# Kernel tuning notes

Measured on AMD Instinct MI355X. Metric: run time of the kernel, lower is better.

Reference implementation:

```python
import jax, jax.numpy as jnp
import numpy as np

IN_COUNT = 1024
OUT_COUNT = 1024
NUM_BASIS = 8
INPUT_ABS_MAX = 1.0
X_MIN = 0.0
X_MAX = 1.0
GAMMA_SCALE = 3.0
BATCH = 4096


def setup_inputs() -> dict:
    key = jax.random.key(0)
    k_x, k_c = jax.random.split(key)
    x = jax.random.normal(k_x, (BATCH, IN_COUNT), dtype=jnp.float32)
    coeffs = 0.01 * jax.random.normal(k_c, (OUT_COUNT, IN_COUNT, NUM_BASIS), dtype=jnp.float32)
    # fixed buffers
    centers_1d = jnp.linspace(X_MIN, X_MAX, NUM_BASIS)
    centers = jnp.broadcast_to(centers_1d[None, :], (IN_COUNT, NUM_BASIS)).astype(jnp.float32)
    delta = (X_MAX - X_MIN) / (NUM_BASIS - 1)
    gamma = GAMMA_SCALE / delta
    slopes = jnp.full((IN_COUNT, NUM_BASIS), gamma, dtype=jnp.float32)
    alpha = jnp.full((IN_COUNT,), (X_MAX - X_MIN) / (2.0 * INPUT_ABS_MAX), dtype=jnp.float32)
    beta = jnp.full((IN_COUNT,), 0.5 * (X_MIN + X_MAX), dtype=jnp.float32)
    return {"x": x, "coeffs": coeffs, "centers": centers, "slopes": slopes, "alpha": alpha, "beta": beta}


def reference(x, coeffs, centers, slopes, alpha, beta):
    # u: (B, in) affine transform with fixed alpha/beta
    u = alpha[None, :] * x + beta[None, :]
    # basis: (B, in, basis) = 0.5*(1+tanh(slope*(u - center)))
    basis = 0.5 * (1.0 + jnp.tanh(slopes[None, :, :] * (u[:, :, None] - centers[None, :, :])))
    # y[b,o] = sum_{i,m} coeffs[o,i,m] * basis[b,i,m]  (fused GEMM over in*basis)
    y = jnp.einsum('bim,oim->bo', basis, coeffs)
    return y
```

## Files before the change

### kernel.cpp

```cpp
#include <hip/hip_runtime.h>
#include <hip/hip_bf16.h>
#include <cstdint>
#include <cstddef>

#define BATCH 4096
#define INC   1024
#define OUTC  1024
#define NB    8
#define KDIM  (INC * NB)

#define BM 256
#define BN 256
#define BKB 64
#define SPLITS 4
#define KZ (KDIM / SPLITS)
#define KSTEPS (KZ / BKB)
#define GRID_BLOCKS ((OUTC / BN) * (BATCH / BM) * SPLITS)
#define FRAG (16 * BKB)

#define EXPAND_BLOCKS  ((BATCH * INC) / 256)
#define QUANT_BLOCKS   OUTC
#define PREP_BLOCKS    (EXPAND_BLOCKS + QUANT_BLOCKS)

typedef int      v4i __attribute__((ext_vector_type(4)));
typedef unsigned v4u __attribute__((ext_vector_type(4)));
typedef char     v8c __attribute__((ext_vector_type(8)));

__device__ __forceinline__ unsigned short f2bf(float f) {
  union { float f; unsigned u; } v; v.f = f;
  unsigned r = v.u + 0x7fffu + ((v.u >> 16) & 1u);
  return (unsigned short)(r >> 16);
}
__device__ __forceinline__ float bf2f(unsigned short h) {
  union { unsigned u; float f; } v; v.u = ((unsigned)h) << 16; return v.f;
}

__global__ __launch_bounds__(256) void prep_kernel(
    const float* __restrict__ x, const float4* __restrict__ coeffs4,
    const float* __restrict__ centers, const float* __restrict__ slopes,
    const float* __restrict__ alpha, const float* __restrict__ beta,
    char* __restrict__ Ai8, int* __restrict__ Ci8i,
    float* __restrict__ maxrow, int* __restrict__ qcsum) {
  const int blk = blockIdx.x;
  const int tid = threadIdx.x;
  if (blk < EXPAND_BLOCKS) {
    const int idx = blk * 256 + tid;
    const int i = idx & (INC - 1);
    const float u = alpha[i] * x[idx] + beta[i];
    const float s0 = slopes[i * NB];
    const float c0 = centers[i * NB];
    const float c1 = centers[i * NB + 1];
    const float L2E2 = 2.8853900817779268f;
    const float a2 = L2E2 * s0;
    float e = __builtin_amdgcn_exp2f(a2 * (c0 - u));
    const float R = __builtin_amdgcn_exp2f(a2 * (c1 - c0));
    v8c q;
#pragma unroll
    for (int m = 0; m < 8; ++m) {
      float basis = __builtin_amdgcn_rcpf(1.0f + e);
      q[m] = (char)(int)rintf(basis * 254.0f - 127.0f);
      e *= R;
    }
    *(v8c*)(Ai8 + (size_t)idx * 8) = q;
  } else {
    const int o = blk - EXPAND_BLOCKS;
    const float4* row = coeffs4 + (size_t)o * (KDIM / 4);
    float4 v[8];
    float m = 0.0f;
#pragma unroll
    for (int j = 0; j < 8; ++j) {
      v[j] = row[tid + 256 * j];
      m = fmaxf(m, fmaxf(fmaxf(fabsf(v[j].x), fabsf(v[j].y)),
                         fmaxf(fabsf(v[j].z), fabsf(v[j].w))));
    }
#pragma unroll
    for (int off = 32; off; off >>= 1) m = fmaxf(m, __shfl_xor(m, off));
    __shared__ float wm[4];
    __shared__ int   wq[4];
    if ((tid & 63) == 0) wm[tid >> 6] = m;
    __syncthreads();
    const float M = fmaxf(fmaxf(fmaxf(wm[0], wm[1]), fmaxf(wm[2], wm[3])), 1e-30f);
    const float s = 127.0f / M;
    int qs = 0;
#pragma unroll
    for (int j = 0; j < 8; ++j) {
      int q0 = (int)rintf(v[j].x * s), q1 = (int)rintf(v[j].y * s);
      int q2 = (int)rintf(v[j].z * s), q3 = (int)rintf(v[j].w * s);
      Ci8i[(size_t)o * (KDIM / 4) + tid + 256 * j] =
          (q0 & 0xFF) | ((q1 & 0xFF) << 8) | ((q2 & 0xFF) << 16) | ((q3 & 0xFF) << 24);
      qs += q0 + q1 + q2 + q3;
    }
#pragma unroll
    for (int off = 32; off; off >>= 1) qs += __shfl_xor(qs, off);
    if ((tid & 63) == 0) wq[tid >> 6] = qs;
    __syncthreads();
    if (tid == 0) { maxrow[o] = M; qcsum[o] = wq[0] + wq[1] + wq[2] + wq[3]; }
  }
}

__global__ __launch_bounds__(512, 2) void gemm_kernel(
    const char* __restrict__ A, const char* __restrict__ C,
    unsigned* __restrict__ partials) {
  __shared__ __align__(16) char As[2][BM * BKB];
  __shared__ __align__(16) char Bs[2][BN * BKB];

  const int id = (blockIdx.x & 7) * (GRID_BLOCKS / 8) + (blockIdx.x >> 3);
  const int z  = id >> 6;
  const int p  = id & 63;
  const int by = p >> 2;
  const int bx = p & 3;
  const int bm0 = by * BM;
  const int bn0 = bx * BN;
  const int kt0 = z * KZ;

  const int tid  = threadIdx.x;
  const int wave = tid >> 6;
  const int lane = tid & 63;
  const int quad = lane >> 4;
  const int lm   = lane & 15;
  const int wm   = (wave >> 2) * 128;
  const int wn   = (wave & 3) * 64;

  const int r4 = lane >> 2;
  const int gg = (lane & 3) ^ ((lane >> 3) & 3);

  const char* pA0 = A + (size_t)(bm0 + wave * 32 + r4) * KDIM + kt0 + gg * 16;
  const char* pB0 = C + (size_t)(bn0 + wave * 32 + r4) * KDIM + kt0 + gg * 16;
  const int lo = wave * 32 * BKB;

  const int kx   = (quad ^ ((lm >> 1) & 3)) * 16;
  const int aoff = (wm + lm) * BKB + kx;
  const int boff = (wn + lm) * BKB + kx;

  v4i acc[8][4] = {};
  v4u g0A0, g0A1, g0B0, g0B1;
  v4u g1A0, g1A1, g1B0, g1B1;

#define GLOAD(A0, A1, B0, B1)                                                \
  {                                                                          \
    A0 = *(const v4u*)(pA0);                                                 \
    A1 = *(const v4u*)(pA0 + (size_t)16 * KDIM);                             \
    B0 = *(const v4u*)(pB0);                                                 \
    B1 = *(const v4u*)(pB0 + (size_t)16 * KDIM);                             \
    pA0 += BKB; pB0 += BKB;                                                  \
  }

#define DSWRITE(SL, A0, A1, B0, B1)                                          \
  {                                                                          \
    *(v4u*)(As[SL] + lo + lane * 16)            = A0;                        \
    *(v4u*)(As[SL] + lo + 16 * BKB + lane * 16) = A1;                        \
    *(v4u*)(Bs[SL] + lo + lane * 16)            = B0;                        \
    *(v4u*)(Bs[SL] + lo + 16 * BKB + lane * 16) = B1;                        \
  }

#define GSTEP(CUR, LA0, LA1, LB0, LB1, WA0, WA1, WB0, WB1, DOGLOAD, DOWRITE, DOBAR) \
  {                                                                          \
    if (DOGLOAD) GLOAD(LA0, LA1, LB0, LB1)                                   \
    const char* cA = As[CUR] + aoff;                                         \
    const char* cB = Bs[CUR] + boff;                                         \
    v4i a[8], b[4];                                                          \
    _Pragma("unroll")                                                        \
    for (int f = 0; f < 4; ++f) a[f] = *(const v4i*)(cA + f * FRAG);         \
    _Pragma("unroll")                                                        \
    for (int f = 0; f < 4; ++f) b[f] = *(const v4i*)(cB + f * FRAG);         \
    _Pragma("unroll")                                                        \
    for (int f = 4; f < 8; ++f) a[f] = *(const v4i*)(cA + f * FRAG);         \
    if (DOWRITE) DSWRITE(CUR ^ 1, WA0, WA1, WB0, WB1)                        \
    __builtin_amdgcn_s_setprio(1);                                           \
    _Pragma("unroll")                                                        \
    for (int fm = 0; fm < 4; ++fm)                                           \
      _Pragma("unroll")                                                      \
      for (int fn = 0; fn < 4; ++fn)                                         \
        acc[fm][fn] = __builtin_amdgcn_mfma_i32_16x16x64_i8(a[fm], b[fn], acc[fm][fn], 0, 0, 0); \
    _Pragma("unroll")                                                        \
    for (int fm = 4; fm < 8; ++fm)                                           \
      _Pragma("unroll")                                                      \
      for (int fn = 0; fn < 4; ++fn)                                         \
        acc[fm][fn] = __builtin_amdgcn_mfma_i32_16x16x64_i8(a[fm], b[fn], acc[fm][fn], 0, 0, 0); \
    __builtin_amdgcn_s_setprio(0);                                           \
    if (DOBAR) __syncthreads();                                              \
  }

  GLOAD(g0A0, g0A1, g0B0, g0B1)
  GLOAD(g1A0, g1A1, g1B0, g1B1)
  DSWRITE(0, g0A0, g0A1, g0B0, g0B1)
  __syncthreads();

  for (int i = 0; i < 15; ++i) {
    GSTEP(0, g0A0, g0A1, g0B0, g0B1, g1A0, g1A1, g1B0, g1B1, true, true, true)
    GSTEP(1, g1A0, g1A1, g1B0, g1B1, g0A0, g0A1, g0B0, g0B1, true, true, true)
  }
  GSTEP(0, g0A0, g0A1, g0B0, g0B1, g1A0, g1A1, g1B0, g1B1, false, true, true)
  GSTEP(1, g1A0, g1A1, g1B0, g1B1, g0A0, g0A1, g0B0, g0B1, false, false, false)
#undef GSTEP
#undef DSWRITE
#undef GLOAD

  unsigned w32[64];
#pragma unroll
  for (int fm = 0; fm < 8; ++fm)
#pragma unroll
    for (int fn = 0; fn < 4; ++fn)
#pragma unroll
      for (int rr = 0; rr < 2; ++rr)
        w32[fm * 8 + fn * 2 + rr] =
            (unsigned)f2bf((float)acc[fm][fn][2 * rr]) |
            ((unsigned)f2bf((float)acc[fm][fn][2 * rr + 1]) << 16);

  unsigned* outp = partials + (((size_t)z * 64 + p) * 8 + wave) * 4096 + lane * 4;
#pragma unroll
  for (int c = 0; c < 16; ++c)
    *(v4u*)(outp + c * 256) = v4u{w32[4 * c], w32[4 * c + 1], w32[4 * c + 2], w32[4 * c + 3]};
}

__global__ __launch_bounds__(256) void reduce_kernel(
    const unsigned* __restrict__ P, const float* __restrict__ maxrow,
    const int* __restrict__ qcsum, float* __restrict__ out) {
  const int blk = blockIdx.x;
  const int p = blk >> 3, w = blk & 7;
  const int by = p >> 2, bx = p & 3;
  const int B0 = by * BM + (w >> 2) * 128;
  const int O0 = bx * BN + (w & 3) * 64;
  const int t = threadIdx.x;
  const int l = t & 63;

  __shared__ float tile[128][65];
  __shared__ float sM[64];
  __shared__ float sQ[64];
  if (t < 64) { sM[t] = maxrow[O0 + t]; sQ[t] = 127.0f * (float)qcsum[O0 + t]; }
  __syncthreads();

  const size_t region = ((size_t)p * 8 + w) * 4096;
  const size_t zs     = (size_t)64 * 8 * 4096;
  float slo[16] = {}, shi[16] = {};
#pragma unroll
  for (int z = 0; z < SPLITS; ++z) {
#pragma unroll
    for (int r = 0; r < 4; ++r) {
      v4u u = *(const v4u*)(P + z * zs + region + ((t >> 6) + r * 4) * 256 + l * 4);
#pragma unroll
      for (int i = 0; i < 4; ++i) {
        slo[r * 4 + i] += bf2f((unsigned short)(u[i] & 0xFFFFu));
        shi[r * 4 + i] += bf2f((unsigned short)(u[i] >> 16));
      }
    }
  }
  const float inv = 1.0f / 32258.0f;
#pragma unroll
  for (int r = 0; r < 4; ++r)
#pragma unroll
    for (int i = 0; i < 4; ++i) {
      const int jj = (t >> 6) * 4 + r * 16 + i;
      const int fm = jj >> 3, fn = (jj >> 1) & 3, rr = jj & 1;
      const int bl = fm * 16 + (l >> 4) * 4 + rr * 2;
      const int ol = fn * 16 + (l & 15);
      const float M = sM[ol], corr = sQ[ol];
      tile[bl][ol]     = M * (slo[r * 4 + i] + corr) * inv;
      tile[bl + 1][ol] = M * (shi[r * 4 + i] + corr) * inv;
    }
  __syncthreads();

  const int row = t >> 1;
  const int c0  = (t & 1) * 32;
  float* op = out + (size_t)(B0 + row) * OUTC + O0 + c0;
#pragma unroll
  for (int i = 0; i < 8; ++i)
    *(float4*)(op + 4 * i) = float4{tile[row][c0 + 4 * i],     tile[row][c0 + 4 * i + 1],
                                    tile[row][c0 + 4 * i + 2], tile[row][c0 + 4 * i + 3]};
}

extern "C" void kernel_launch(void* const* d_in, const int* in_sizes, int n_in,
                              void* d_out, int out_size, void* d_ws, size_t ws_size,
                              hipStream_t stream) {
  const float* x       = (const float*)d_in[0];
  const float* coeffs  = (const float*)d_in[1];
  const float* centers = (const float*)d_in[2];
  const float* slopes  = (const float*)d_in[3];
  const float* alpha   = (const float*)d_in[4];
  const float* beta    = (const float*)d_in[5];
  float* out = (float*)d_out;

  const size_t a_bytes    = (size_t)BATCH * KDIM;
  const size_t c_bytes    = (size_t)OUTC * KDIM;
  const size_t stat_bytes = OUTC * sizeof(float);
  const size_t qcs_bytes  = OUTC * sizeof(int);
  const size_t part_bytes = (size_t)SPLITS * BATCH * OUTC * 2;
  if (ws_size < a_bytes + c_bytes + stat_bytes + qcs_bytes + part_bytes) return;

  char*  Ai8    = (char*)d_ws;
  char*  Ci8    = Ai8 + a_bytes;
  float* maxrow = (float*)(Ci8 + c_bytes);
  int*   qcsum  = (int*)((char*)maxrow + stat_bytes);
  unsigned* parts = (unsigned*)((char*)qcsum + qcs_bytes);

  prep_kernel<<<PREP_BLOCKS, 256, 0, stream>>>(
      x, (const float4*)coeffs, centers, slopes, alpha, beta,
      Ai8, (int*)Ci8, maxrow, qcsum);

  gemm_kernel<<<GRID_BLOCKS, 512, 0, stream>>>(Ai8, Ci8, parts);

  reduce_kernel<<<64 * 8, 256, 0, stream>>>(parts, maxrow, qcsum, out);
}
```

Measured before the change: 152.6 us.

## Load MFMA fragments directly from global memory, bypassing LDS staging

Removes the shared-memory double buffer and barriers in the int8 GEMM. Each wave now loads its A and B fragments straight from global memory into register double buffers, interleaved with MFMA blocks. This eliminates LDS writes, reads and syncs, but every wave re-fetches data that was previously shared across the block. That raises L2/L1 traffic and register pressure.

```diff
diff --git a/kernel.cpp b/kernel.cpp
--- a/kernel.cpp
+++ b/kernel.cpp
@@ -16,7 +16,6 @@
 #define KZ (KDIM / SPLITS)
 #define KSTEPS (KZ / BKB)
 #define GRID_BLOCKS ((OUTC / BN) * (BATCH / BM) * SPLITS)
-#define FRAG (16 * BKB)
 
 #define EXPAND_BLOCKS  ((BATCH * INC) / 256)
 #define QUANT_BLOCKS   OUTC
@@ -75,11 +74,11 @@
     }
 #pragma unroll
     for (int off = 32; off; off >>= 1) m = fmaxf(m, __shfl_xor(m, off));
-    __shared__ float wm[4];
-    __shared__ int   wq[4];
-    if ((tid & 63) == 0) wm[tid >> 6] = m;
+    __shared__ float wm_[4];
+    __shared__ int   wq_[4];
+    if ((tid & 63) == 0) wm_[tid >> 6] = m;
     __syncthreads();
-    const float M = fmaxf(fmaxf(fmaxf(wm[0], wm[1]), fmaxf(wm[2], wm[3])), 1e-30f);
+    const float M = fmaxf(fmaxf(fmaxf(wm_[0], wm_[1]), fmaxf(wm_[2], wm_[3])), 1e-30f);
     const float s = 127.0f / M;
     int qs = 0;
 #pragma unroll
@@ -92,18 +91,15 @@
     }
 #pragma unroll
     for (int off = 32; off; off >>= 1) qs += __shfl_xor(qs, off);
-    if ((tid & 63) == 0) wq[tid >> 6] = qs;
+    if ((tid & 63) == 0) wq_[tid >> 6] = qs;
     __syncthreads();
-    if (tid == 0) { maxrow[o] = M; qcsum[o] = wq[0] + wq[1] + wq[2] + wq[3]; }
+    if (tid == 0) { maxrow[o] = M; qcsum[o] = wq_[0] + wq_[1] + wq_[2] + wq_[3]; }
   }
 }
 
 __global__ __launch_bounds__(512, 2) void gemm_kernel(
     const char* __restrict__ A, const char* __restrict__ C,
     unsigned* __restrict__ partials) {
-  __shared__ __align__(16) char As[2][BM * BKB];
-  __shared__ __align__(16) char Bs[2][BN * BKB];
-
   const int id = (blockIdx.x & 7) * (GRID_BLOCKS / 8) + (blockIdx.x >> 3);
   const int z  = id >> 6;
   const int p  = id & 63;
@@ -121,80 +117,44 @@
   const int wm   = (wave >> 2) * 128;
   const int wn   = (wave & 3) * 64;
 
-  const int r4 = lane >> 2;
-  const int gg = (lane & 3) ^ ((lane >> 3) & 3);
-
-  const char* pA0 = A + (size_t)(bm0 + wave * 32 + r4) * KDIM + kt0 + gg * 16;
-  const char* pB0 = C + (size_t)(bn0 + wave * 32 + r4) * KDIM + kt0 + gg * 16;
-  const int lo = wave * 32 * BKB;
-
-  const int kx   = (quad ^ ((lm >> 1) & 3)) * 16;
-  const int aoff = (wm + lm) * BKB + kx;
-  const int boff = (wn + lm) * BKB + kx;
+  const char* aBase = A + (size_t)(bm0 + wm + lm) * KDIM + kt0 + quad * 16;
+  const char* bBase = C + (size_t)(bn0 + wn + lm) * KDIM + kt0 + quad * 16;
 
   v4i acc[8][4] = {};
-  v4u g0A0, g0A1, g0B0, g0B1;
-  v4u g1A0, g1A1, g1B0, g1B1;
-
-#define GLOAD(A0, A1, B0, B1)                                                \
+  v4i xa[8], xb[4], ya[8], yb[4];
+
+#define LOADF(AV, BV, T)                                                     \
   {                                                                          \
-    A0 = *(const v4u*)(pA0);                                                 \
-    A1 = *(const v4u*)(pA0 + (size_t)16 * KDIM);                             \
-    B0 = *(const v4u*)(pB0);                                                 \
-    B1 = *(const v4u*)(pB0 + (size_t)16 * KDIM);                             \
-    pA0 += BKB; pB0 += BKB;                                                  \
-  }
-
-#define DSWRITE(SL, A0, A1, B0, B1)                                          \
+    _Pragma("unroll")                                                        \
+    for (int f = 0; f < 8; ++f)                                              \
+      AV[f] = *(const v4i*)(aBase + (size_t)f * (16 * KDIM) + (size_t)(T) * BKB); \
+    _Pragma("unroll")                                                        \
+    for (int f = 0; f < 4; ++f)                                              \
+      BV[f] = *(const v4i*)(bBase + (size_t)f * (16 * KDIM) + (size_t)(T) * BKB); \
+  }
+
+#define MFMA32(AV, BV)                                                       \
   {                                                                          \
-    *(v4u*)(As[SL] + lo + lane * 16)            = A0;                        \
-    *(v4u*)(As[SL] + lo + 16 * BKB + lane * 16) = A1;                        \
-    *(v4u*)(Bs[SL] + lo + lane * 16)            = B0;                        \
-    *(v4u*)(Bs[SL] + lo + 16 * BKB + lane * 16) = B1;                        \
-  }
-
-#define GSTEP(CUR, LA0, LA1, LB0, LB1, WA0, WA1, WB0, WB1, DOGLOAD, DOWRITE, DOBAR) \
-  {                                                                          \
-    if (DOGLOAD) GLOAD(LA0, LA1, LB0, LB1)                                   \
-    const char* cA = As[CUR] + aoff;                                         \
-    const char* cB = Bs[CUR] + boff;                                         \
-    v4i a[8], b[4];                                                          \
     _Pragma("unroll")                                                        \
-    for (int f = 0; f < 4; ++f) a[f] = *(const v4i*)(cA + f * FRAG);         \
-    _Pragma("unroll")                                                        \
-    for (int f = 0; f < 4; ++f) b[f] = *(const v4i*)(cB + f * FRAG);         \
-    _Pragma("unroll")                                                        \
-    for (int f = 4; f < 8; ++f) a[f] = *(const v4i*)(cA + f * FRAG);         \
-    if (DOWRITE) DSWRITE(CUR ^ 1, WA0, WA1, WB0, WB1)                        \
-    __builtin_amdgcn_s_setprio(1);                                           \
-    _Pragma("unroll")                                                        \
-    for (int fm = 0; fm < 4; ++fm)                                           \
+    for (int fm = 0; fm < 8; ++fm)                                           \
       _Pragma("unroll")                                                      \
       for (int fn = 0; fn < 4; ++fn)                                         \
-        acc[fm][fn] = __builtin_amdgcn_mfma_i32_16x16x64_i8(a[fm], b[fn], acc[fm][fn], 0, 0, 0); \
-    _Pragma("unroll")                                                        \
-    for (int fm = 4; fm < 8; ++fm)                                           \
-      _Pragma("unroll")                                                      \
-      for (int fn = 0; fn < 4; ++fn)                                         \
-        acc[fm][fn] = __builtin_amdgcn_mfma_i32_16x16x64_i8(a[fm], b[fn], acc[fm][fn], 0, 0, 0); \
-    __builtin_amdgcn_s_setprio(0);                                           \
-    if (DOBAR) __syncthreads();                                              \
-  }
-
-  GLOAD(g0A0, g0A1, g0B0, g0B1)
-  GLOAD(g1A0, g1A1, g1B0, g1B1)
-  DSWRITE(0, g0A0, g0A1, g0B0, g0B1)
-  __syncthreads();
-
+        acc[fm][fn] = __builtin_amdgcn_mfma_i32_16x16x64_i8(AV[fm], BV[fn], acc[fm][fn], 0, 0, 0); \
+  }
+
+  LOADF(xa, xb, 0)
   for (int i = 0; i < 15; ++i) {
-    GSTEP(0, g0A0, g0A1, g0B0, g0B1, g1A0, g1A1, g1B0, g1B1, true, true, true)
-    GSTEP(1, g1A0, g1A1, g1B0, g1B1, g0A0, g0A1, g0B0, g0B1, true, true, true)
-  }
-  GSTEP(0, g0A0, g0A1, g0B0, g0B1, g1A0, g1A1, g1B0, g1B1, false, true, true)
-  GSTEP(1, g1A0, g1A1, g1B0, g1B1, g0A0, g0A1, g0B0, g0B1, false, false, false)
-#undef GSTEP
-#undef DSWRITE
-#undef GLOAD
+    const int t = 2 * i;
+    LOADF(ya, yb, t + 1)
+    MFMA32(xa, xb)
+    LOADF(xa, xb, t + 2)
+    MFMA32(ya, yb)
+  }
+  LOADF(ya, yb, 31)
+  MFMA32(xa, xb)
+  MFMA32(ya, yb)
+#undef MFMA32
+#undef LOADF
 
   unsigned w32[64];
 #pragma unroll
```

After: 211.7 us. 38.7% more time.
